# Performance work log

Measured on AMD Instinct MI355X. Metric: run time of the kernel, lower is better.

## Reference

```python
import jax, jax.numpy as jnp
import numpy as np

ALPHA = 0.2  # LeakyReLU negative slope
NEG_BIG = -9e15


def setup_inputs() -> dict:
    key = jax.random.key(0)
    k1, k2, k3, k4 = jax.random.split(key, 4)
    B, N, Fin, Fout = 16, 1024, 256, 256
    h = jax.random.normal(k1, (B, N, Fin), dtype=jnp.float32)
    adj = jax.random.randint(k2, (B, N, N), 0, 2, dtype=jnp.int32)
    # xavier_uniform with gain=1.414
    def xavier(k, shape, gain=1.414):
        fan_in, fan_out = shape[0], shape[1]
        bound = gain * np.sqrt(6.0 / (fan_in + fan_out))
        return jax.random.uniform(k, shape, jnp.float32, -bound, bound)
    W = xavier(k3, (Fin, Fout))
    a = xavier(k4, (2 * Fout, 1))
    return {"h": h, "adj": adj, "W": W, "a": a}


def reference(h, adj, W, a):
    # h: [B,N,Fin], adj: [B,N,N], W: [Fin,Fout], a: [2*Fout,1]
    Fout = W.shape[1]
    Wh = jnp.einsum('bnf,fo->bno', h, W)                      # [B,N,Fout]
    a1, a2 = a[:Fout, 0], a[Fout:, 0]                          # [Fout], [Fout]
    # e_ij = leakyrelu(Wh_i . a1 + Wh_j . a2) -- outer sum, no O(N^2*F) tensor
    f1 = Wh @ a1                                               # [B,N]
    f2 = Wh @ a2                                               # [B,N]
    e = jax.nn.leaky_relu(f1[:, :, None] + f2[:, None, :], negative_slope=ALPHA)
    attention = jnp.where(adj > 0, e, jnp.float32(NEG_BIG))    # [B,N,N]
    attention = jax.nn.softmax(attention, axis=2)
    h_prime = jnp.einsum('bij,bjo->bio', attention, Wh)        # [B,N,Fout]
    return jax.nn.elu(h_prime)
```

## Files before the change

kernel.cpp:

```cpp
#include <hip/hip_runtime.h>
#include <hip/hip_bf16.h>

#define Bsz 16
#define Nn  1024
#define Ff  256
#define ALPHA 0.2f
#define NEG_BIG -9.0e15f
#define LOG2E 1.44269504f

typedef __attribute__((ext_vector_type(8))) short short8;
typedef __attribute__((ext_vector_type(4))) float f32x4;
typedef __attribute__((ext_vector_type(4))) unsigned short ushort4_t;

__device__ __forceinline__ unsigned short f2bf(float x) {
    union { __hip_bfloat16 b; unsigned short u; } cv;
    cv.b = __float2bfloat16(x);
    return cv.u;
}

__device__ __forceinline__ float exp2_fast(float x) {
#if __has_builtin(__builtin_amdgcn_exp2f)
    return __builtin_amdgcn_exp2f(x);
#else
    return exp2f(x);
#endif
}

__device__ __forceinline__ float rcp_fast(float x) {
#if __has_builtin(__builtin_amdgcn_rcpf)
    return __builtin_amdgcn_rcpf(x);
#else
    return 1.f / x;
#endif
}

__global__ __launch_bounds__(256) void gat_prep(
    const float* __restrict__ W, const float* __restrict__ a,
    float* __restrict__ w1, float* __restrict__ w2)
{
    const int t = threadIdx.x, w = t >> 6, ln = t & 63;
    __shared__ float a1s[Ff], a2s[Ff];
    a1s[t] = a[t];
    a2s[t] = a[Ff + t];
    __syncthreads();
    const int f = blockIdx.x * 4 + w;
    float s1 = 0.f, s2 = 0.f;
    #pragma unroll
    for (int c = 0; c < 4; c++) {
        const int o = ln + 64 * c;
        const float wv = W[(size_t)f * Ff + o];
        s1 += wv * a1s[o];
        s2 += wv * a2s[o];
    }
    #pragma unroll
    for (int off = 1; off < 64; off <<= 1) {
        s1 += __shfl_xor(s1, off, 64);
        s2 += __shfl_xor(s2, off, 64);
    }
    if (ln == 0) { w1[f] = s1; w2[f] = s2; }
}

__global__ __launch_bounds__(256) void pack_f(
    const float* __restrict__ h, const float* __restrict__ W,
    const float* __restrict__ w1, const float* __restrict__ w2,
    unsigned short* __restrict__ hK, unsigned short* __restrict__ WK,
    float* __restrict__ f1, float* __restrict__ f2)
{
    __shared__ __align__(16) float tile[32][260];
    const int id = blockIdx.x, t = threadIdx.x, w = t >> 6, ln = t & 63;
    const bool isH = (id < 512);
    const float* src;
    unsigned short* dst;
    int grow0 = 0;
    if (isH) {
        const int b = id >> 5, kt = id & 31;
        grow0 = b * Nn + kt * 32;
        src = h + (size_t)grow0 * Ff;
        dst = hK + ((size_t)(b * 32 + kt)) * 8192;
    } else {
        const int ft = id - 512;
        src = W + (size_t)ft * 32 * Ff;
        dst = WK + (size_t)ft * 8192;
    }
    #pragma unroll
    for (int rr = 0; rr < 8; rr++) {
        const int row = rr * 4 + w;
        const int col = ln * 4;
        *(float4*)&tile[row][col] = *(const float4*)&src[row * Ff + col];
    }
    __syncthreads();

    unsigned* d32 = (unsigned*)dst;
    #pragma unroll
    for (int k = 0; k < 16; k++) {
        const int fidx = k * 256 + t;
        const int o = fidx >> 4, q = fidx & 15;
        const unsigned lo = f2bf(tile[2 * q][o]);
        const unsigned hi = f2bf(tile[2 * q + 1][o]);
        d32[fidx] = lo | (hi << 16);
    }

    if (isH) {
        float w1r[4], w2r[4];
        #pragma unroll
        for (int c = 0; c < 4; c++) {
            w1r[c] = w1[ln + 64 * c];
            w2r[c] = w2[ln + 64 * c];
        }
        #pragma unroll
        for (int rr = 0; rr < 8; rr++) {
            const int row = rr * 4 + w;
            float s1 = 0.f, s2 = 0.f;
            #pragma unroll
            for (int c = 0; c < 4; c++) {
                const float hv = tile[row][ln + 64 * c];
                s1 += hv * w1r[c];
                s2 += hv * w2r[c];
            }
            #pragma unroll
            for (int off = 1; off < 64; off <<= 1) {
                s1 += __shfl_xor(s1, off, 64);
                s2 += __shfl_xor(s2, off, 64);
            }
            if (ln == 0) { f1[grow0 + row] = s1; f2[grow0 + row] = s2; }
        }
    }
}

#define TI 32
__global__ __launch_bounds__(1024, 8) void gat_attn(
    const int* __restrict__ adj,
    const float* __restrict__ f1, const float* __restrict__ f2,
    const unsigned short* __restrict__ hK, const unsigned short* __restrict__ WK,
    float* __restrict__ out)
{
    __shared__ __align__(16) unsigned short pbf[TI * 1024];
    __shared__ __align__(16) float ss[TI];
    const int t = threadIdx.x, w = t >> 6, ln = t & 63;
    const int m = ln & 15, quad = ln >> 4;
    const int bid = blockIdx.x;
    const int b  = 2 * (bid & 7) + ((bid >> 3) & 1);
    const int i0 = (bid >> 4) * TI;

    const int r0 = 2 * w, r1 = r0 + 1;
    const int grb = b * Nn + i0 + r0;
    const int* aptr = adj + (size_t)grb * Nn;
    int4 av0[4], av1[4];
    #pragma unroll
    for (int c = 0; c < 4; c++) {
        av0[c] = *(const int4*)&aptr[c * 256 + 4 * ln];
        av1[c] = *(const int4*)&aptr[Nn + c * 256 + 4 * ln];
    }

    float4 f2r[4];
    #pragma unroll
    for (int c = 0; c < 4; c++)
        f2r[c] = *(const float4*)&f2[b * Nn + 256 * c + 4 * ln];

    float mx2 = fmaxf(fmaxf(f2r[0].x, f2r[0].y), fmaxf(f2r[0].z, f2r[0].w));
    #pragma unroll
    for (int c = 1; c < 4; c++)
        mx2 = fmaxf(mx2, fmaxf(fmaxf(f2r[c].x, f2r[c].y), fmaxf(f2r[c].z, f2r[c].w)));
    #pragma unroll
    for (int off = 1; off < 64; off <<= 1)
        mx2 = fmaxf(mx2, __shfl_xor(mx2, off, 64));

    #pragma unroll
    for (int c = 0; c < 4; c++) {
        f2r[c].x *= LOG2E; f2r[c].y *= LOG2E;
        f2r[c].z *= LOG2E; f2r[c].w *= LOG2E;
    }

    const float fi0 = f1[grb], fi1 = f1[grb + 1];
    float q0 = fi0 + mx2; q0 = fmaxf(q0, ALPHA * q0);
    float q1 = fi1 + mx2; q1 = fmaxf(q1, ALPHA * q1);
    const float mx0L = q0 * LOG2E, mx1L = q1 * LOG2E;
    const float fi0L = fi0 * LOG2E, fi1L = fi1 * LOG2E;
    const int sw0 = (r0 & 7) << 3, sw1 = (r1 & 7) << 3;

    float s0 = 0.f, s1 = 0.f;
    #pragma unroll
    for (int c = 0; c < 4; c++) {
        const float4 fv = f2r[c];
        float x, p00, p01, p02, p03, p10, p11, p12, p13;
        x = fi0L + fv.x; x = fmaxf(x, ALPHA * x); p00 = exp2_fast(x - mx0L); p00 = av0[c].x > 0 ? p00 : 0.f;
        x = fi0L + fv.y; x = fmaxf(x, ALPHA * x); p01 = exp2_fast(x - mx0L); p01 = av0[c].y > 0 ? p01 : 0.f;
        x = fi0L + fv.z; x = fmaxf(x, ALPHA * x); p02 = exp2_fast(x - mx0L); p02 = av0[c].z > 0 ? p02 : 0.f;
        x = fi0L + fv.w; x = fmaxf(x, ALPHA * x); p03 = exp2_fast(x - mx0L); p03 = av0[c].w > 0 ? p03 : 0.f;
        x = fi1L + fv.x; x = fmaxf(x, ALPHA * x); p10 = exp2_fast(x - mx1L); p10 = av1[c].x > 0 ? p10 : 0.f;
        x = fi1L + fv.y; x = fmaxf(x, ALPHA * x); p11 = exp2_fast(x - mx1L); p11 = av1[c].y > 0 ? p11 : 0.f;
        x = fi1L + fv.z; x = fmaxf(x, ALPHA * x); p12 = exp2_fast(x - mx1L); p12 = av1[c].z > 0 ? p12 : 0.f;
        x = fi1L + fv.w; x = fmaxf(x, ALPHA * x); p13 = exp2_fast(x - mx1L); p13 = av1[c].w > 0 ? p13 : 0.f;
        s0 += (p00 + p01) + (p02 + p03);
        s1 += (p10 + p11) + (p12 + p13);
        const int j = 256 * c + 4 * ln;
        ushort4_t v0 = { f2bf(p00), f2bf(p01), f2bf(p02), f2bf(p03) };
        ushort4_t v1 = { f2bf(p10), f2bf(p11), f2bf(p12), f2bf(p13) };
        *(ushort4_t*)&pbf[r0 * 1024 + (j ^ sw0)] = v0;
        *(ushort4_t*)&pbf[r1 * 1024 + (j ^ sw1)] = v1;
    }
    #pragma unroll
    for (int off = 1; off < 64; off <<= 1) {
        s0 += __shfl_xor(s0, off, 64);
        s1 += __shfl_xor(s1, off, 64);
    }
    if (ln == 0) { ss[r0] = s0; ss[r1] = s1; }
    __syncthreads();

    const int n0 = w * 16;
    const unsigned short* hKb = hK + (size_t)b * 32 * 8192;
    const int arow0 = m * 1024, arow1 = (16 + m) * 1024;
    const int asw = (m & 7) << 3;
    #define AF0(kt) (*(const short8*)&pbf[arow0 + ((((kt) * 32) + quad * 8) ^ asw)])
    #define AF1(kt) (*(const short8*)&pbf[arow1 + ((((kt) * 32) + quad * 8) ^ asw)])
    #define BF(kt)  (*(const short8*)&hKb[(size_t)(kt) * 8192 + (n0 + m) * 32 + quad * 8])

    f32x4 acc0 = {0.f,0.f,0.f,0.f}, acc1 = acc0;
    short8 a0c = AF0(0), a1c = AF1(0);
    short8 bc = BF(0), bn = BF(1);
    #pragma unroll
    for (int kt = 0; kt < 32; kt++) {
        short8 bnn = bc, a0n = a0c, a1n = a1c;
        if (kt + 2 < 32) bnn = BF(kt + 2);
        if (kt + 1 < 32) { a0n = AF0(kt + 1); a1n = AF1(kt + 1); }
        acc0 = __builtin_amdgcn_mfma_f32_16x16x32_bf16(a0c, bc, acc0, 0, 0, 0);
        acc1 = __builtin_amdgcn_mfma_f32_16x16x32_bf16(a1c, bc, acc1, 0, 0, 0);
        a0c = a0n; a1c = a1n; bc = bn; bn = bnn;
    }

    const f32x4 sv0 = *(const f32x4*)&ss[quad * 4];
    const f32x4 sv1 = *(const f32x4*)&ss[16 + quad * 4];

    __syncthreads();
    #pragma unroll
    for (int reg = 0; reg < 4; reg++) {
        const float i0s = rcp_fast(fmaxf(sv0[reg], 1e-30f));
        const float i1s = rcp_fast(fmaxf(sv1[reg], 1e-30f));
        pbf[(quad * 4 + reg) * 264 + n0 + m]      = f2bf(acc0[reg] * i0s);
        pbf[(16 + quad * 4 + reg) * 264 + n0 + m] = f2bf(acc1[reg] * i1s);
    }
    __syncthreads();

    #define GA0(kt) (*(const short8*)&pbf[m * 264 + (kt) * 32 + quad * 8])
    #define GA1(kt) (*(const short8*)&pbf[(16 + m) * 264 + (kt) * 32 + quad * 8])
    #define WB(kt)  (*(const short8*)&WK[(size_t)(kt) * 8192 + (n0 + m) * 32 + quad * 8])

    f32x4 c0 = {0.f,0.f,0.f,0.f}, c1 = c0;
    short8 ga0 = GA0(0), ga1 = GA1(0), wb = WB(0);
    #pragma unroll
    for (int kt = 0; kt < 8; kt++) {
        short8 ga0n = ga0, ga1n = ga1, wbn = wb;
        if (kt + 1 < 8) { ga0n = GA0(kt + 1); ga1n = GA1(kt + 1); wbn = WB(kt + 1); }
        c0 = __builtin_amdgcn_mfma_f32_16x16x32_bf16(ga0, wb, c0, 0, 0, 0);
        c1 = __builtin_amdgcn_mfma_f32_16x16x32_bf16(ga1, wb, c1, 0, 0, 0);
        ga0 = ga0n; ga1 = ga1n; wb = wbn;
    }
    const size_t ob = (size_t)(b * Nn) + i0;
    #pragma unroll
    for (int reg = 0; reg < 4; reg++) {
        float v;
        v = c0[reg]; v = v > 0.f ? v : (__expf(v) - 1.f);
        out[(ob + quad * 4 + reg) * Ff + n0 + m] = v;
        v = c1[reg]; v = v > 0.f ? v : (__expf(v) - 1.f);
        out[(ob + 16 + quad * 4 + reg) * Ff + n0 + m] = v;
    }
}

extern "C" void kernel_launch(void* const* d_in, const int* in_sizes, int n_in,
                              void* d_out, int out_size, void* d_ws, size_t ws_size,
                              hipStream_t stream)
{
    const void* h   = d_in[0];
    const void* adj = d_in[1];
    const void* W   = d_in[2];
    const void* a   = d_in[3];
    for (int i = 0; i < n_in; i++) {
        if      (in_sizes[i] == Bsz * Nn * Ff) h   = d_in[i];
        else if (in_sizes[i] == Bsz * Nn * Nn) adj = d_in[i];
        else if (in_sizes[i] == Ff * Ff)       W   = d_in[i];
        else if (in_sizes[i] == 2 * Ff)        a   = d_in[i];
    }
    float* out = (float*)d_out;

    char*  wsb = (char*)d_ws;
    float* w1  = (float*)wsb;
    float* w2  = w1 + Ff;
    float* f1  = (float*)(wsb + 4096);
    float* f2  = f1 + Bsz * Nn;
    unsigned short* hK = (unsigned short*)(wsb + 4096 + 2 * 65536);
    unsigned short* WK = hK + (size_t)Bsz * 32 * 8192;

    gat_prep<<<64, 256, 0, stream>>>((const float*)W, (const float*)a, w1, w2);
    pack_f<<<520, 256, 0, stream>>>((const float*)h, (const float*)W, w1, w2, hK, WK, f1, f2);
    gat_attn<<<Bsz * (Nn / TI), 1024, 0, stream>>>((const int*)adj, f1, f2, hK, WK, out);
}
```

Measured before the change: 143.7 us.

## Pre-pack adjacency into bitmasks and raise MFMA wave priority

Adds a pass, merged into the prep kernel, that compresses the int32 adjacency matrix into 64-bit ballot bitmasks. The attention kernel then reads compact masks, made wave-uniform with readfirstlane and applied through inverse ballot, instead of int4 adjacency loads. The aim is to make the adjacency cheaper to consume, but the full 64MB int32 adjacency is still read once per call, in the extra pass. The change also issues the first B-fragment loads before the barrier and sets s_setprio around the MFMA loops.

```diff
diff --git a/kernel.cpp b/kernel.cpp
--- a/kernel.cpp
+++ b/kernel.cpp
@@ -5,7 +5,6 @@
 #define Nn  1024
 #define Ff  256
 #define ALPHA 0.2f
-#define NEG_BIG -9.0e15f
 #define LOG2E 1.44269504f
 
 typedef __attribute__((ext_vector_type(8))) short short8;
@@ -34,30 +33,70 @@
 #endif
 }
 
-__global__ __launch_bounds__(256) void gat_prep(
+__device__ __forceinline__ unsigned long long rfl64(unsigned long long v) {
+    unsigned lo = __builtin_amdgcn_readfirstlane((unsigned)v);
+    unsigned hi = __builtin_amdgcn_readfirstlane((unsigned)(v >> 32));
+    return ((unsigned long long)hi << 32) | lo;
+}
+
+__device__ __forceinline__ float maskf(float p, unsigned long long ms, int ln) {
+#if __has_builtin(__builtin_amdgcn_inverse_ballot_w64)
+    return __builtin_amdgcn_inverse_ballot_w64(ms) ? p : 0.f;
+#else
+    return ((ms >> ln) & 1ull) ? p : 0.f;
+#endif
+}
+
+__global__ __launch_bounds__(256) void prep_pack(
     const float* __restrict__ W, const float* __restrict__ a,
-    float* __restrict__ w1, float* __restrict__ w2)
+    const int* __restrict__ adj,
+    float* __restrict__ w1, float* __restrict__ w2,
+    unsigned long long* __restrict__ abit)
 {
     const int t = threadIdx.x, w = t >> 6, ln = t & 63;
     __shared__ float a1s[Ff], a2s[Ff];
-    a1s[t] = a[t];
-    a2s[t] = a[Ff + t];
-    __syncthreads();
-    const int f = blockIdx.x * 4 + w;
-    float s1 = 0.f, s2 = 0.f;
-    #pragma unroll
-    for (int c = 0; c < 4; c++) {
-        const int o = ln + 64 * c;
-        const float wv = W[(size_t)f * Ff + o];
-        s1 += wv * a1s[o];
-        s2 += wv * a2s[o];
-    }
-    #pragma unroll
-    for (int off = 1; off < 64; off <<= 1) {
-        s1 += __shfl_xor(s1, off, 64);
-        s2 += __shfl_xor(s2, off, 64);
-    }
-    if (ln == 0) { w1[f] = s1; w2[f] = s2; }
+    if (blockIdx.x < 64) {
+        a1s[t] = a[t];
+        a2s[t] = a[Ff + t];
+        __syncthreads();
+        const int f = blockIdx.x * 4 + w;
+        float s1 = 0.f, s2 = 0.f;
+        #pragma unroll
+        for (int c = 0; c < 4; c++) {
+            const int o = ln + 64 * c;
+            const float wv = W[(size_t)f * Ff + o];
+            s1 += wv * a1s[o];
+            s2 += wv * a2s[o];
+        }
+        #pragma unroll
+        for (int off = 1; off < 64; off <<= 1) {
+            s1 += __shfl_xor(s1, off, 64);
+            s2 += __shfl_xor(s2, off, 64);
+        }
+        if (ln == 0) { w1[f] = s1; w2[f] = s2; }
+        return;
+    }
+    const int id2 = blockIdx.x - 64;
+    const int row0 = id2 * 8 + 2 * w;
+    const int* ap = adj + (size_t)row0 * Nn;
+    int4 vv[8];
+    #pragma unroll
+    for (int u = 0; u < 8; u++)
+        vv[u] = *(const int4*)&ap[(u >> 2) * Nn + (u & 3) * 256 + 4 * ln];
+    #pragma unroll
+    for (int u = 0; u < 8; u++) {
+        const unsigned long long b0 = __ballot(vv[u].x > 0);
+        const unsigned long long b1 = __ballot(vv[u].y > 0);
+        const unsigned long long b2 = __ballot(vv[u].z > 0);
+        const unsigned long long b3 = __ballot(vv[u].w > 0);
+        if (ln == 0) {
+            const size_t base = (size_t)(row0 + (u >> 2)) * 16 + (u & 3) * 4;
+            abit[base]     = b0;
+            abit[base + 1] = b1;
+            abit[base + 2] = b2;
+            abit[base + 3] = b3;
+        }
+    }
 }
 
 __global__ __launch_bounds__(256) void pack_f(
@@ -129,7 +168,7 @@
 
 #define TI 32
 __global__ __launch_bounds__(1024, 8) void gat_attn(
-    const int* __restrict__ adj,
+    const unsigned long long* __restrict__ abit,
     const float* __restrict__ f1, const float* __restrict__ f2,
     const unsigned short* __restrict__ hK, const unsigned short* __restrict__ WK,
     float* __restrict__ out)
@@ -144,13 +183,7 @@
 
     const int r0 = 2 * w, r1 = r0 + 1;
     const int grb = b * Nn + i0 + r0;
-    const int* aptr = adj + (size_t)grb * Nn;
-    int4 av0[4], av1[4];
-    #pragma unroll
-    for (int c = 0; c < 4; c++) {
-        av0[c] = *(const int4*)&aptr[c * 256 + 4 * ln];
-        av1[c] = *(const int4*)&aptr[Nn + c * 256 + 4 * ln];
-    }
+    const unsigned long long* ab = abit + (size_t)grb * 16;
 
     float4 f2r[4];
     #pragma unroll
@@ -178,19 +211,35 @@
     const float fi0L = fi0 * LOG2E, fi1L = fi1 * LOG2E;
     const int sw0 = (r0 & 7) << 3, sw1 = (r1 & 7) << 3;
 
+    ulonglong2 qa0 = *(const ulonglong2*)&ab[0];
+    ulonglong2 qb0 = *(const ulonglong2*)&ab[2];
+    ulonglong2 qc0 = *(const ulonglong2*)&ab[16];
+    ulonglong2 qd0 = *(const ulonglong2*)&ab[18];
+
     float s0 = 0.f, s1 = 0.f;
     #pragma unroll
     for (int c = 0; c < 4; c++) {
+        ulonglong2 qa1 = qa0, qb1 = qb0, qc1 = qc0, qd1 = qd0;
+        if (c < 3) {
+            qa1 = *(const ulonglong2*)&ab[4 * (c + 1)];
+            qb1 = *(const ulonglong2*)&ab[4 * (c + 1) + 2];
+            qc1 = *(const ulonglong2*)&ab[16 + 4 * (c + 1)];
+            qd1 = *(const ulonglong2*)&ab[16 + 4 * (c + 1) + 2];
+        }
+        const unsigned long long m00 = rfl64(qa0.x), m01 = rfl64(qa0.y);
+        const unsigned long long m02 = rfl64(qb0.x), m03 = rfl64(qb0.y);
+        const unsigned long long m10 = rfl64(qc0.x), m11 = rfl64(qc0.y);
+        const unsigned long long m12 = rfl64(qd0.x), m13 = rfl64(qd0.y);
         const float4 fv = f2r[c];
         float x, p00, p01, p02, p03, p10, p11, p12, p13;
-        x = fi0L + fv.x; x = fmaxf(x, ALPHA * x); p00 = exp2_fast(x - mx0L); p00 = av0[c].x > 0 ? p00 : 0.f;
-        x = fi0L + fv.y; x = fmaxf(x, ALPHA * x); p01 = exp2_fast(x - mx0L); p01 = av0[c].y > 0 ? p01 : 0.f;
-        x = fi0L + fv.z; x = fmaxf(x, ALPHA * x); p02 = exp2_fast(x - mx0L); p02 = av0[c].z > 0 ? p02 : 0.f;
-        x = fi0L + fv.w; x = fmaxf(x, ALPHA * x); p03 = exp2_fast(x - mx0L); p03 = av0[c].w > 0 ? p03 : 0.f;
-        x = fi1L + fv.x; x = fmaxf(x, ALPHA * x); p10 = exp2_fast(x - mx1L); p10 = av1[c].x > 0 ? p10 : 0.f;
-        x = fi1L + fv.y; x = fmaxf(x, ALPHA * x); p11 = exp2_fast(x - mx1L); p11 = av1[c].y > 0 ? p11 : 0.f;
-        x = fi1L + fv.z; x = fmaxf(x, ALPHA * x); p12 = exp2_fast(x - mx1L); p12 = av1[c].z > 0 ? p12 : 0.f;
-        x = fi1L + fv.w; x = fmaxf(x, ALPHA * x); p13 = exp2_fast(x - mx1L); p13 = av1[c].w > 0 ? p13 : 0.f;
+        x = fi0L + fv.x; x = fmaxf(x, ALPHA * x); p00 = maskf(exp2_fast(x - mx0L), m00, ln);
+        x = fi0L + fv.y; x = fmaxf(x, ALPHA * x); p01 = maskf(exp2_fast(x - mx0L), m01, ln);
+        x = fi0L + fv.z; x = fmaxf(x, ALPHA * x); p02 = maskf(exp2_fast(x - mx0L), m02, ln);
+        x = fi0L + fv.w; x = fmaxf(x, ALPHA * x); p03 = maskf(exp2_fast(x - mx0L), m03, ln);
+        x = fi1L + fv.x; x = fmaxf(x, ALPHA * x); p10 = maskf(exp2_fast(x - mx1L), m10, ln);
+        x = fi1L + fv.y; x = fmaxf(x, ALPHA * x); p11 = maskf(exp2_fast(x - mx1L), m11, ln);
+        x = fi1L + fv.z; x = fmaxf(x, ALPHA * x); p12 = maskf(exp2_fast(x - mx1L), m12, ln);
+        x = fi1L + fv.w; x = fmaxf(x, ALPHA * x); p13 = maskf(exp2_fast(x - mx1L), m13, ln);
         s0 += (p00 + p01) + (p02 + p03);
         s1 += (p10 + p11) + (p12 + p13);
         const int j = 256 * c + 4 * ln;
@@ -198,6 +247,7 @@
         ushort4_t v1 = { f2bf(p10), f2bf(p11), f2bf(p12), f2bf(p13) };
         *(ushort4_t*)&pbf[r0 * 1024 + (j ^ sw0)] = v0;
         *(ushort4_t*)&pbf[r1 * 1024 + (j ^ sw1)] = v1;
+        qa0 = qa1; qb0 = qb1; qc0 = qc1; qd0 = qd1;
     }
     #pragma unroll
     for (int off = 1; off < 64; off <<= 1) {
@@ -205,7 +255,6 @@
         s1 += __shfl_xor(s1, off, 64);
     }
     if (ln == 0) { ss[r0] = s0; ss[r1] = s1; }
-    __syncthreads();
 
     const int n0 = w * 16;
     const unsigned short* hKb = hK + (size_t)b * 32 * 8192;
@@ -215,9 +264,12 @@
     #define AF1(kt) (*(const short8*)&pbf[arow1 + ((((kt) * 32) + quad * 8) ^ asw)])
     #define BF(kt)  (*(const short8*)&hKb[(size_t)(kt) * 8192 + (n0 + m) * 32 + quad * 8])
 
+    short8 bc = BF(0), bn = BF(1);
+    __syncthreads();
+
     f32x4 acc0 = {0.f,0.f,0.f,0.f}, acc1 = acc0;
     short8 a0c = AF0(0), a1c = AF1(0);
-    short8 bc = BF(0), bn = BF(1);
+    __builtin_amdgcn_s_setprio(1);
     #pragma unroll
     for (int kt = 0; kt < 32; kt++) {
         short8 bnn = bc, a0n = a0c, a1n = a1c;
@@ -227,6 +279,7 @@
         acc1 = __builtin_amdgcn_mfma_f32_16x16x32_bf16(a1c, bc, acc1, 0, 0, 0);
         a0c = a0n; a1c = a1n; bc = bn; bn = bnn;
     }
+    __builtin_amdgcn_s_setprio(0);
 
     const f32x4 sv0 = *(const f32x4*)&ss[quad * 4];
     const f32x4 sv1 = *(const f32x4*)&ss[16 + quad * 4];
@@ -247,6 +300,7 @@
 
     f32x4 c0 = {0.f,0.f,0.f,0.f}, c1 = c0;
     short8 ga0 = GA0(0), ga1 = GA1(0), wb = WB(0);
+    __builtin_amdgcn_s_setprio(1);
     #pragma unroll
     for (int kt = 0; kt < 8; kt++) {
         short8 ga0n = ga0, ga1n = ga1, wbn = wb;
@@ -255,6 +309,7 @@
         c1 = __builtin_amdgcn_mfma_f32_16x16x32_bf16(ga1, wb, c1, 0, 0, 0);
         ga0 = ga0n; ga1 = ga1n; wb = wbn;
     }
+    __builtin_amdgcn_s_setprio(0);
     const size_t ob = (size_t)(b * Nn) + i0;
     #pragma unroll
     for (int reg = 0; reg < 4; reg++) {
@@ -289,8 +344,10 @@
     float* f2  = f1 + Bsz * Nn;
     unsigned short* hK = (unsigned short*)(wsb + 4096 + 2 * 65536);
     unsigned short* WK = hK + (size_t)Bsz * 32 * 8192;
-
-    gat_prep<<<64, 256, 0, stream>>>((const float*)W, (const float*)a, w1, w2);
+    unsigned long long* abit = (unsigned long long*)(wsb + 12 * 1024 * 1024);
+
+    prep_pack<<<64 + 2048, 256, 0, stream>>>((const float*)W, (const float*)a,
+                                             (const int*)adj, w1, w2, abit);
     pack_f<<<520, 256, 0, stream>>>((const float*)h, (const float*)W, w1, w2, hK, WK, f1, f2);
-    gat_attn<<<Bsz * (Nn / TI), 1024, 0, stream>>>((const int*)adj, f1, f2, hK, WK, out);
-}
+    gat_attn<<<Bsz * (Nn / TI), 1024, 0, stream>>>(abit, f1, f2, hK, WK, out);
+}
```

Result: no change. 143.0 us (-0.5%).

## Fuse prep into pack kernel, deepen B-operand prefetch and raise MFMA priority

Applied to the files above, without the earlier changes.

Removes the separate gat_prep launch. Each of the 512 pack blocks (now 1024 threads) recomputes W·a1 and W·a2 into shared memory, and the first 16 blocks also pack W into WK. This saves one kernel launch and the dependency between launches, at the cost of redundant W reads in every block. In the attention kernel the first global B-operand loads are hoisted ahead of the __syncthreads barriers, the hK prefetch depth goes from two to four, and the MFMA loops are wrapped in s_setprio. The exp2 is also made conditional on the adjacency mask.

```diff
diff --git a/kernel.cpp b/kernel.cpp
--- a/kernel.cpp
+++ b/kernel.cpp
@@ -5,7 +5,6 @@
 #define Nn  1024
 #define Ff  256
 #define ALPHA 0.2f
-#define NEG_BIG -9.0e15f
 #define LOG2E 1.44269504f
 
 typedef __attribute__((ext_vector_type(8))) short short8;
@@ -34,116 +33,110 @@
 #endif
 }
 
-__global__ __launch_bounds__(256) void gat_prep(
-    const float* __restrict__ W, const float* __restrict__ a,
-    float* __restrict__ w1, float* __restrict__ w2)
-{
-    const int t = threadIdx.x, w = t >> 6, ln = t & 63;
-    __shared__ float a1s[Ff], a2s[Ff];
-    a1s[t] = a[t];
-    a2s[t] = a[Ff + t];
-    __syncthreads();
-    const int f = blockIdx.x * 4 + w;
-    float s1 = 0.f, s2 = 0.f;
-    #pragma unroll
-    for (int c = 0; c < 4; c++) {
-        const int o = ln + 64 * c;
-        const float wv = W[(size_t)f * Ff + o];
-        s1 += wv * a1s[o];
-        s2 += wv * a2s[o];
-    }
-    #pragma unroll
-    for (int off = 1; off < 64; off <<= 1) {
-        s1 += __shfl_xor(s1, off, 64);
-        s2 += __shfl_xor(s2, off, 64);
-    }
-    if (ln == 0) { w1[f] = s1; w2[f] = s2; }
-}
-
-__global__ __launch_bounds__(256) void pack_f(
+__global__ __launch_bounds__(1024, 4) void k_pack(
     const float* __restrict__ h, const float* __restrict__ W,
-    const float* __restrict__ w1, const float* __restrict__ w2,
+    const float* __restrict__ a,
     unsigned short* __restrict__ hK, unsigned short* __restrict__ WK,
     float* __restrict__ f1, float* __restrict__ f2)
 {
-    __shared__ __align__(16) float tile[32][260];
-    const int id = blockIdx.x, t = threadIdx.x, w = t >> 6, ln = t & 63;
-    const bool isH = (id < 512);
-    const float* src;
-    unsigned short* dst;
-    int grow0 = 0;
-    if (isH) {
-        const int b = id >> 5, kt = id & 31;
-        grow0 = b * Nn + kt * 32;
-        src = h + (size_t)grow0 * Ff;
-        dst = hK + ((size_t)(b * 32 + kt)) * 8192;
-    } else {
-        const int ft = id - 512;
-        src = W + (size_t)ft * 32 * Ff;
-        dst = WK + (size_t)ft * 8192;
-    }
-    #pragma unroll
-    for (int rr = 0; rr < 8; rr++) {
-        const int row = rr * 4 + w;
-        const int col = ln * 4;
-        *(float4*)&tile[row][col] = *(const float4*)&src[row * Ff + col];
-    }
-    __syncthreads();
-
-    unsigned* d32 = (unsigned*)dst;
-    #pragma unroll
-    for (int k = 0; k < 16; k++) {
-        const int fidx = k * 256 + t;
+    __shared__ __align__(16) float tile[32][258];
+    __shared__ float w1s[Ff], w2s[Ff];
+    const int bid = blockIdx.x, t = threadIdx.x, w = t >> 6, ln = t & 63;
+
+    const int grow0 = bid * 32;
+    const float* src = h + (size_t)grow0 * Ff;
+    const int row = t >> 5, col = (t & 31) * 8;
+    const float4 va = *(const float4*)&src[row * Ff + col];
+    const float4 vb = *(const float4*)&src[row * Ff + col + 4];
+
+    {
+        const int f = t >> 2, q = t & 3;
+        const float4* wr  = (const float4*)(W + (size_t)f * Ff + q * 64);
+        const float4* a1p = (const float4*)(a + q * 64);
+        const float4* a2p = (const float4*)(a + Ff + q * 64);
+        float s1 = 0.f, s2 = 0.f;
+        #pragma unroll
+        for (int i = 0; i < 16; i++) {
+            const float4 wv = wr[i];
+            const float4 x1 = a1p[i], x2 = a2p[i];
+            s1 += wv.x * x1.x + wv.y * x1.y + wv.z * x1.z + wv.w * x1.w;
+            s2 += wv.x * x2.x + wv.y * x2.y + wv.z * x2.z + wv.w * x2.w;
+        }
+        s1 += __shfl_xor(s1, 1, 64); s1 += __shfl_xor(s1, 2, 64);
+        s2 += __shfl_xor(s2, 1, 64); s2 += __shfl_xor(s2, 2, 64);
+        if (q == 0) { w1s[f] = s1; w2s[f] = s2; }
+    }
+
+    {
+        float2* tr = (float2*)&tile[row][col];
+        tr[0] = make_float2(va.x, va.y);
+        tr[1] = make_float2(va.z, va.w);
+        tr[2] = make_float2(vb.x, vb.y);
+        tr[3] = make_float2(vb.z, vb.w);
+    }
+    __syncthreads();
+
+    unsigned* d32 = (unsigned*)(hK + (size_t)bid * 8192);
+    #pragma unroll
+    for (int k = 0; k < 4; k++) {
+        const int fidx = k * 1024 + t;
         const int o = fidx >> 4, q = fidx & 15;
-        const unsigned lo = f2bf(tile[2 * q][o]);
-        const unsigned hi = f2bf(tile[2 * q + 1][o]);
-        d32[fidx] = lo | (hi << 16);
-    }
-
-    if (isH) {
-        float w1r[4], w2r[4];
+        d32[fidx] = (unsigned)f2bf(tile[2 * q][o]) | ((unsigned)f2bf(tile[2 * q + 1][o]) << 16);
+    }
+    #pragma unroll
+    for (int rr = 0; rr < 2; rr++) {
+        const int r = 2 * w + rr;
+        float s1 = 0.f, s2 = 0.f;
         #pragma unroll
         for (int c = 0; c < 4; c++) {
-            w1r[c] = w1[ln + 64 * c];
-            w2r[c] = w2[ln + 64 * c];
-        }
-        #pragma unroll
-        for (int rr = 0; rr < 8; rr++) {
-            const int row = rr * 4 + w;
-            float s1 = 0.f, s2 = 0.f;
-            #pragma unroll
-            for (int c = 0; c < 4; c++) {
-                const float hv = tile[row][ln + 64 * c];
-                s1 += hv * w1r[c];
-                s2 += hv * w2r[c];
-            }
-            #pragma unroll
-            for (int off = 1; off < 64; off <<= 1) {
-                s1 += __shfl_xor(s1, off, 64);
-                s2 += __shfl_xor(s2, off, 64);
-            }
-            if (ln == 0) { f1[grow0 + row] = s1; f2[grow0 + row] = s2; }
-        }
-    }
-}
-
-#define TI 32
-__global__ __launch_bounds__(1024, 8) void gat_attn(
+            const int o = ln + 64 * c;
+            const float hv = tile[r][o];
+            s1 += hv * w1s[o];
+            s2 += hv * w2s[o];
+        }
+        #pragma unroll
+        for (int off = 1; off < 64; off <<= 1) {
+            s1 += __shfl_xor(s1, off, 64);
+            s2 += __shfl_xor(s2, off, 64);
+        }
+        if (ln == 0) { f1[grow0 + r] = s1; f2[grow0 + r] = s2; }
+    }
+    if (bid < 16) {
+        const int ft = bid >> 1, half = bid & 1;
+        __syncthreads();
+        const int r16 = t >> 6, c4 = (t & 63) * 4;
+        const float4 wv = *(const float4*)&W[(size_t)(ft * 32 + half * 16 + r16) * Ff + c4];
+        float2* tr = (float2*)&tile[r16][c4];
+        tr[0] = make_float2(wv.x, wv.y);
+        tr[1] = make_float2(wv.z, wv.w);
+        __syncthreads();
+        unsigned* wd = (unsigned*)(WK + (size_t)ft * 8192);
+        #pragma unroll
+        for (int k = 0; k < 2; k++) {
+            const int j = k * 1024 + t;
+            const int o = j >> 3, ql = j & 7;
+            wd[o * 16 + half * 8 + ql] =
+                (unsigned)f2bf(tile[2 * ql][o]) | ((unsigned)f2bf(tile[2 * ql + 1][o]) << 16);
+        }
+    }
+}
+
+__global__ __launch_bounds__(1024, 8) void k_attn(
     const int* __restrict__ adj,
     const float* __restrict__ f1, const float* __restrict__ f2,
     const unsigned short* __restrict__ hK, const unsigned short* __restrict__ WK,
     float* __restrict__ out)
 {
-    __shared__ __align__(16) unsigned short pbf[TI * 1024];
-    __shared__ __align__(16) float ss[TI];
+    __shared__ __align__(16) unsigned short pbf[32 * 1024];
+    __shared__ __align__(16) float ss[32];
     const int t = threadIdx.x, w = t >> 6, ln = t & 63;
     const int m = ln & 15, quad = ln >> 4;
     const int bid = blockIdx.x;
-    const int b  = 2 * (bid & 7) + ((bid >> 3) & 1);
-    const int i0 = (bid >> 4) * TI;
+    const int b2 = 2 * (bid & 7) + ((bid >> 3) & 1);
+    const int i0 = (bid >> 4) * 32;
 
     const int r0 = 2 * w, r1 = r0 + 1;
-    const int grb = b * Nn + i0 + r0;
+    const int grb = b2 * Nn + i0 + r0;
     const int* aptr = adj + (size_t)grb * Nn;
     int4 av0[4], av1[4];
     #pragma unroll
@@ -155,7 +148,7 @@
     float4 f2r[4];
     #pragma unroll
     for (int c = 0; c < 4; c++)
-        f2r[c] = *(const float4*)&f2[b * Nn + 256 * c + 4 * ln];
+        f2r[c] = *(const float4*)&f2[b2 * Nn + 256 * c + 4 * ln];
 
     float mx2 = fmaxf(fmaxf(f2r[0].x, f2r[0].y), fmaxf(f2r[0].z, f2r[0].w));
     #pragma unroll
@@ -183,14 +176,14 @@
     for (int c = 0; c < 4; c++) {
         const float4 fv = f2r[c];
         float x, p00, p01, p02, p03, p10, p11, p12, p13;
-        x = fi0L + fv.x; x = fmaxf(x, ALPHA * x); p00 = exp2_fast(x - mx0L); p00 = av0[c].x > 0 ? p00 : 0.f;
-        x = fi0L + fv.y; x = fmaxf(x, ALPHA * x); p01 = exp2_fast(x - mx0L); p01 = av0[c].y > 0 ? p01 : 0.f;
-        x = fi0L + fv.z; x = fmaxf(x, ALPHA * x); p02 = exp2_fast(x - mx0L); p02 = av0[c].z > 0 ? p02 : 0.f;
-        x = fi0L + fv.w; x = fmaxf(x, ALPHA * x); p03 = exp2_fast(x - mx0L); p03 = av0[c].w > 0 ? p03 : 0.f;
-        x = fi1L + fv.x; x = fmaxf(x, ALPHA * x); p10 = exp2_fast(x - mx1L); p10 = av1[c].x > 0 ? p10 : 0.f;
-        x = fi1L + fv.y; x = fmaxf(x, ALPHA * x); p11 = exp2_fast(x - mx1L); p11 = av1[c].y > 0 ? p11 : 0.f;
-        x = fi1L + fv.z; x = fmaxf(x, ALPHA * x); p12 = exp2_fast(x - mx1L); p12 = av1[c].z > 0 ? p12 : 0.f;
-        x = fi1L + fv.w; x = fmaxf(x, ALPHA * x); p13 = exp2_fast(x - mx1L); p13 = av1[c].w > 0 ? p13 : 0.f;
+        x = fi0L + fv.x; x = fmaxf(x, ALPHA * x); p00 = av0[c].x > 0 ? exp2_fast(x - mx0L) : 0.f;
+        x = fi0L + fv.y; x = fmaxf(x, ALPHA * x); p01 = av0[c].y > 0 ? exp2_fast(x - mx0L) : 0.f;
+        x = fi0L + fv.z; x = fmaxf(x, ALPHA * x); p02 = av0[c].z > 0 ? exp2_fast(x - mx0L) : 0.f;
+        x = fi0L + fv.w; x = fmaxf(x, ALPHA * x); p03 = av0[c].w > 0 ? exp2_fast(x - mx0L) : 0.f;
+        x = fi1L + fv.x; x = fmaxf(x, ALPHA * x); p10 = av1[c].x > 0 ? exp2_fast(x - mx1L) : 0.f;
+        x = fi1L + fv.y; x = fmaxf(x, ALPHA * x); p11 = av1[c].y > 0 ? exp2_fast(x - mx1L) : 0.f;
+        x = fi1L + fv.z; x = fmaxf(x, ALPHA * x); p12 = av1[c].z > 0 ? exp2_fast(x - mx1L) : 0.f;
+        x = fi1L + fv.w; x = fmaxf(x, ALPHA * x); p13 = av1[c].w > 0 ? exp2_fast(x - mx1L) : 0.f;
         s0 += (p00 + p01) + (p02 + p03);
         s1 += (p10 + p11) + (p12 + p13);
         const int j = 256 * c + 4 * ln;
@@ -205,28 +198,32 @@
         s1 += __shfl_xor(s1, off, 64);
     }
     if (ln == 0) { ss[r0] = s0; ss[r1] = s1; }
-    __syncthreads();
 
     const int n0 = w * 16;
-    const unsigned short* hKb = hK + (size_t)b * 32 * 8192;
+    const unsigned short* hKb = hK + (size_t)b2 * 32 * 8192;
     const int arow0 = m * 1024, arow1 = (16 + m) * 1024;
     const int asw = (m & 7) << 3;
     #define AF0(kt) (*(const short8*)&pbf[arow0 + ((((kt) * 32) + quad * 8) ^ asw)])
     #define AF1(kt) (*(const short8*)&pbf[arow1 + ((((kt) * 32) + quad * 8) ^ asw)])
     #define BF(kt)  (*(const short8*)&hKb[(size_t)(kt) * 8192 + (n0 + m) * 32 + quad * 8])
 
-    f32x4 acc0 = {0.f,0.f,0.f,0.f}, acc1 = acc0;
+    short8 bq0 = BF(0), bq1 = BF(1), bq2 = BF(2), bq3 = BF(3);
+    __syncthreads();
+
+    f32x4 acc0 = {0.f, 0.f, 0.f, 0.f}, acc1 = acc0;
     short8 a0c = AF0(0), a1c = AF1(0);
-    short8 bc = BF(0), bn = BF(1);
+    __builtin_amdgcn_s_setprio(1);
     #pragma unroll
     for (int kt = 0; kt < 32; kt++) {
-        short8 bnn = bc, a0n = a0c, a1n = a1c;
-        if (kt + 2 < 32) bnn = BF(kt + 2);
+        short8 bnew = bq0, a0n = a0c, a1n = a1c;
+        if (kt + 4 < 32) bnew = BF(kt + 4);
         if (kt + 1 < 32) { a0n = AF0(kt + 1); a1n = AF1(kt + 1); }
-        acc0 = __builtin_amdgcn_mfma_f32_16x16x32_bf16(a0c, bc, acc0, 0, 0, 0);
-        acc1 = __builtin_amdgcn_mfma_f32_16x16x32_bf16(a1c, bc, acc1, 0, 0, 0);
-        a0c = a0n; a1c = a1n; bc = bn; bn = bnn;
-    }
+        acc0 = __builtin_amdgcn_mfma_f32_16x16x32_bf16(a0c, bq0, acc0, 0, 0, 0);
+        acc1 = __builtin_amdgcn_mfma_f32_16x16x32_bf16(a1c, bq0, acc1, 0, 0, 0);
+        a0c = a0n; a1c = a1n;
+        bq0 = bq1; bq1 = bq2; bq2 = bq3; bq3 = bnew;
+    }
+    __builtin_amdgcn_s_setprio(0);
 
     const f32x4 sv0 = *(const f32x4*)&ss[quad * 4];
     const f32x4 sv1 = *(const f32x4*)&ss[16 + quad * 4];
@@ -239,23 +236,28 @@
         pbf[(quad * 4 + reg) * 264 + n0 + m]      = f2bf(acc0[reg] * i0s);
         pbf[(16 + quad * 4 + reg) * 264 + n0 + m] = f2bf(acc1[reg] * i1s);
     }
-    __syncthreads();
 
     #define GA0(kt) (*(const short8*)&pbf[m * 264 + (kt) * 32 + quad * 8])
     #define GA1(kt) (*(const short8*)&pbf[(16 + m) * 264 + (kt) * 32 + quad * 8])
     #define WB(kt)  (*(const short8*)&WK[(size_t)(kt) * 8192 + (n0 + m) * 32 + quad * 8])
 
-    f32x4 c0 = {0.f,0.f,0.f,0.f}, c1 = c0;
-    short8 ga0 = GA0(0), ga1 = GA1(0), wb = WB(0);
+    short8 wbc = WB(0), wbn = WB(1);
+    __syncthreads();
+
+    f32x4 c0 = {0.f, 0.f, 0.f, 0.f}, c1 = c0;
+    short8 ga0 = GA0(0), ga1 = GA1(0);
+    __builtin_amdgcn_s_setprio(1);
     #pragma unroll
     for (int kt = 0; kt < 8; kt++) {
-        short8 ga0n = ga0, ga1n = ga1, wbn = wb;
-        if (kt + 1 < 8) { ga0n = GA0(kt + 1); ga1n = GA1(kt + 1); wbn = WB(kt + 1); }
-        c0 = __builtin_amdgcn_mfma_f32_16x16x32_bf16(ga0, wb, c0, 0, 0, 0);
-        c1 = __builtin_amdgcn_mfma_f32_16x16x32_bf16(ga1, wb, c1, 0, 0, 0);
-        ga0 = ga0n; ga1 = ga1n; wb = wbn;
-    }
-    const size_t ob = (size_t)(b * Nn) + i0;
+        short8 ga0n = ga0, ga1n = ga1, wnew = wbc;
+        if (kt + 2 < 8) wnew = WB(kt + 2);
+        if (kt + 1 < 8) { ga0n = GA0(kt + 1); ga1n = GA1(kt + 1); }
+        c0 = __builtin_amdgcn_mfma_f32_16x16x32_bf16(ga0, wbc, c0, 0, 0, 0);
+        c1 = __builtin_amdgcn_mfma_f32_16x16x32_bf16(ga1, wbc, c1, 0, 0, 0);
+        ga0 = ga0n; ga1 = ga1n; wbc = wbn; wbn = wnew;
+    }
+    __builtin_amdgcn_s_setprio(0);
+    const size_t ob = (size_t)(b2 * Nn) + i0;
     #pragma unroll
     for (int reg = 0; reg < 4; reg++) {
         float v;
@@ -280,17 +282,14 @@
         else if (in_sizes[i] == Ff * Ff)       W   = d_in[i];
         else if (in_sizes[i] == 2 * Ff)        a   = d_in[i];
     }
-    float* out = (float*)d_out;
-
-    char*  wsb = (char*)d_ws;
-    float* w1  = (float*)wsb;
-    float* w2  = w1 + Ff;
-    float* f1  = (float*)(wsb + 4096);
-    float* f2  = f1 + Bsz * Nn;
-    unsigned short* hK = (unsigned short*)(wsb + 4096 + 2 * 65536);
+    char* wsb = (char*)d_ws;
+    float* f1 = (float*)wsb;
+    float* f2 = (float*)(wsb + 65536);
+    unsigned short* hK = (unsigned short*)(wsb + 2 * 65536);
     unsigned short* WK = hK + (size_t)Bsz * 32 * 8192;
 
-    gat_prep<<<64, 256, 0, stream>>>((const float*)W, (const float*)a, w1, w2);
-    pack_f<<<520, 256, 0, stream>>>((const float*)h, (const float*)W, w1, w2, hK, WK, f1, f2);
-    gat_attn<<<Bsz * (Nn / TI), 1024, 0, stream>>>((const int*)adj, f1, f2, hK, WK, out);
-}
+    k_pack<<<512, 1024, 0, stream>>>((const float*)h, (const float*)W,
+                                     (const float*)a, hK, WK, f1, f2);
+    k_attn<<<512, 1024, 0, stream>>>((const int*)adj, f1, f2, hK, WK,
+                                     (float*)d_out);
+}
```

New measurement: 179.1 us. 24.7% more time.
